# Kernel tuning notes

Hardware: AMD Instinct MI355X
Metric: run time of the kernel (lower is better)

## Reference

```python
import jax, jax.numpy as jnp
import numpy as np


def setup_inputs() -> dict:
    key = jax.random.key(0)
    ks = jax.random.split(key, 4)
    B, T, E, H = 4, 4096, 512, 64
    x = jax.random.normal(ks[0], (B, T, E), dtype=jnp.float32)
    s = 1.0 / np.sqrt(E)
    Wq = jax.random.normal(ks[1], (E, H), dtype=jnp.float32) * s
    Wk = jax.random.normal(ks[2], (E, H), dtype=jnp.float32) * s
    Wv = jax.random.normal(ks[3], (E, H), dtype=jnp.float32) * s
    bq = jnp.zeros((H,), dtype=jnp.float32)
    bk = jnp.zeros((H,), dtype=jnp.float32)
    bv = jnp.zeros((H,), dtype=jnp.float32)
    return {"x": x, "Wq": Wq, "bq": bq, "Wk": Wk, "bk": bk, "Wv": Wv, "bv": bv}


def reference(x, Wq, bq, Wk, bk, Wv, bv):
    # Single-head causal attention (masked=True path; dropout off / eval mode).
    B, T, E = x.shape
    H = Wq.shape[1]
    q = x @ Wq + bq                      # [B,T,H]
    k = x @ Wk + bk                      # [B,T,H]
    v = x @ Wv + bv                      # [B,T,H]
    scale = jnp.asarray(H, x.dtype) ** -0.5
    w = jnp.einsum('bqh,bkh->bqk', q, k) * scale   # [B,T,T]
    causal = jnp.tril(jnp.ones((T, T), dtype=bool))
    w = jnp.where(causal, w, jnp.asarray(-jnp.inf, w.dtype))
    w = jax.nn.softmax(w, axis=-1)
    out = jnp.einsum('bqk,bkh->bqh', w, v)          # [B,T,H]
    return out
```

## Files before the change

kernel.cpp:

```cpp
#include <hip/hip_runtime.h>
#include <math.h>

#define B_SZ   4
#define T_SEQ  4096
#define E_DIM  512
#define H_DIM  64
#define AW     8
#define XSTR   520
#define QSCALE 0.180336878f

typedef float f32x4 __attribute__((ext_vector_type(4)));
typedef short s16x4 __attribute__((ext_vector_type(4)));
typedef short s16x8 __attribute__((ext_vector_type(8)));
typedef unsigned int u32x4 __attribute__((ext_vector_type(4)));

static __device__ __forceinline__ unsigned short f2bf(float f) {
    union { float f; unsigned int u; } c; c.f = f;
    return (unsigned short)((c.u + 0x7fffu + ((c.u >> 16) & 1u)) >> 16);
}

static __device__ __forceinline__ float exp2f_hw(float x) {
    return __builtin_amdgcn_exp2f(x);
}

static __device__ __forceinline__ unsigned int pack_bf16(float a, float b) {
    unsigned int ua = __builtin_bit_cast(unsigned int, a) + 0x8000u;
    unsigned int ub = __builtin_bit_cast(unsigned int, b) + 0x8000u;
    return __builtin_amdgcn_perm(ub, ua, 0x07060302u);
}

__global__ __launch_bounds__(256) void wconv(
    const float* __restrict__ Wq, const float* __restrict__ Wk, const float* __restrict__ Wv,
    unsigned short* __restrict__ Wf)
{
    const int fid  = blockIdx.x * 256 + threadIdx.x;
    const int nt   = fid >> 10;
    const int kc32 = (fid >> 6) & 15;
    const int lane = fid & 63;
    const int l15  = lane & 15, g = lane >> 4;
    const int col  = nt * 16 + l15;
    const int m    = col >> 6, h = col & 63;
    const float* src = (m == 0) ? Wq : (m == 1) ? Wk : Wv;
    const float sc = (m == 0) ? QSCALE : 1.0f;
    const int k0 = kc32 * 32 + 4 * g;
    s16x8 o;
    #pragma unroll
    for (int j = 0; j < 4; ++j) {
        o[j]     = (short)f2bf(src[(k0 + j) * H_DIM + h] * sc);
        o[4 + j] = (short)f2bf(src[(k0 + 16 + j) * H_DIM + h] * sc);
    }
    *(s16x8*)(Wf + (long long)fid * 8) = o;
}

__global__ __launch_bounds__(256) void qkv_mfma(
    const float* __restrict__ x, const unsigned short* __restrict__ Wf,
    const float* __restrict__ bq, const float* __restrict__ bk, const float* __restrict__ bv,
    unsigned short* __restrict__ qf, unsigned short* __restrict__ kf,
    unsigned short* __restrict__ vf)
{
    __shared__ unsigned short Xf[2][16 * XSTR];
    __shared__ unsigned short Wout[192][36];

    const int t = threadIdx.x, wv = t >> 6, l = t & 63, l15 = l & 15, g = l >> 4;
    const long long row0 = (long long)blockIdx.x * 32;

    const float* xbase = x + row0 * E_DIM;
    #pragma unroll
    for (int i = 0; i < 16; ++i) {
        const int n = t + 256 * i;
        const int r = n >> 7;
        const int c = (n & 127) * 4;
        const f32x4 xv = *(const f32x4*)(xbase + r * E_DIM + c);
        const int rs = r >> 4, rr = r & 15;
        const int kc32 = c >> 5, rem = c & 31;
        const int gg = (rem & 15) >> 2, half = rem >> 4;
        unsigned int* dst = (unsigned int*)&Xf[rs][kc32 * XSTR + (rr + 16 * gg) * 8 + half * 4];
        dst[0] = pack_bf16(xv[0], xv[1]);
        dst[1] = pack_bf16(xv[2], xv[3]);
    }
    __syncthreads();

    f32x4 acc[2][3];
    #pragma unroll
    for (int rs = 0; rs < 2; ++rs)
        #pragma unroll
        for (int i = 0; i < 3; ++i) acc[rs][i] = (f32x4){0.f, 0.f, 0.f, 0.f};

    #pragma unroll
    for (int kc32 = 0; kc32 < 16; ++kc32) {
        const s16x8 xf0 = *(const s16x8*)&Xf[0][kc32 * XSTR + l * 8];
        const s16x8 xf1 = *(const s16x8*)&Xf[1][kc32 * XSTR + l * 8];
        #pragma unroll
        for (int i = 0; i < 3; ++i) {
            const int nt = wv + 4 * i;
            const s16x8 wf = *(const s16x8*)(Wf + (long long)((nt * 16 + kc32) * 64 + l) * 8);
            acc[0][i] = __builtin_amdgcn_mfma_f32_16x16x32_bf16(wf, xf0, acc[0][i], 0, 0, 0);
            acc[1][i] = __builtin_amdgcn_mfma_f32_16x16x32_bf16(wf, xf1, acc[1][i], 0, 0, 0);
        }
    }

    #pragma unroll
    for (int i = 0; i < 3; ++i) {
        const int nt = wv + 4 * i;
        const float* bsrc = (i == 0) ? bq : (i == 1) ? bk : bv;
        const float bscale = (i == 0) ? QSCALE : 1.0f;
        const f32x4 bb = *(const f32x4*)(bsrc + wv * 16 + 4 * g);
        #pragma unroll
        for (int rs = 0; rs < 2; ++rs)
            #pragma unroll
            for (int r = 0; r < 4; ++r)
                Wout[nt * 16 + 4 * g + r][16 * rs + l15] = f2bf(acc[rs][i][r] + bb[r] * bscale);
    }
    __syncthreads();

    #pragma unroll
    for (int rt = 0; rt < 2; ++rt) {
        const long long qt = (long long)blockIdx.x * 2 + rt;

        if (t < 128) {
            const int hc = t >> 6, ll = t & 63, p15 = ll & 15, pg = (ll >> 4);
            s16x8 o;
            #pragma unroll
            for (int j = 0; j < 4; ++j) {
                o[j]     = (short)Wout[32 * hc + 4 * pg + j][16 * rt + p15];
                o[4 + j] = (short)Wout[32 * hc + 16 + 4 * pg + j][16 * rt + p15];
            }
            *(s16x8*)(qf + qt * 1024 + hc * 512 + ll * 8) = o;
        } else {
            const int tt = t - 128, half = tt >> 6, ll = tt & 63, p15 = ll & 15, pg = (ll >> 4);
            s16x8 o;
            #pragma unroll
            for (int j = 0; j < 4; ++j) {
                o[j]     = (short)Wout[64 + 32 * half + 4 * pg + j][16 * rt + p15];
                o[4 + j] = (short)Wout[64 + 32 * half + 16 + 4 * pg + j][16 * rt + p15];
            }
            *(s16x8*)(kf + qt * 1024 + half * 512 + ll * 8) = o;
        }

        {
            const int hc = t >> 6, ll = t & 63, p15 = ll & 15, pg = (ll >> 4);
            const long long ktg = qt >> 2;
            const int half = (int)((qt >> 1) & 1), pi = (int)(qt & 1);
            s16x4 o;
            #pragma unroll
            for (int j = 0; j < 4; ++j)
                o[j] = (short)Wout[128 + hc * 16 + p15][16 * rt + 4 * pg + j];
            *(s16x4*)(vf + ktg * 4096 + hc * 1024 + half * 512 + ll * 8 + pi * 4) = o;
        }
    }
}

__global__ __launch_bounds__(512, 2) void attn(
    const unsigned short* __restrict__ qf,
    const unsigned short* __restrict__ kf,
    const unsigned short* __restrict__ vf,
    float* __restrict__ out)
{
    __shared__ float Osh[AW][64][33];
    __shared__ float msh[AW][32];
    __shared__ float lsh[AW][32];

    const int t = threadIdx.x, wv = t >> 6, l = t & 63, l15 = l & 15, g = l >> 4;

    const int bid = blockIdx.x;
    const int xcd = bid & 7;
    const int b   = xcd >> 1;
    const int u   = (bid >> 3) * 2 + (xcd & 1);
    const int qi  = 127 - u;
    const int q0  = qi * 32;
    const int adiag = (q0 + 31) >> 6;

    const unsigned short* kfb = kf + (long long)b * 64 * 4096 + l * 8;
    const unsigned short* vfb = vf + (long long)b * 64 * 4096 + l * 8;

    s16x8 Qf[2][2];
    #pragma unroll
    for (int s = 0; s < 2; ++s) {
        const unsigned short* qp = qf + ((long long)b * 256 + qi * 2 + s) * 1024 + l * 8;
        Qf[s][0] = *(const s16x8*)qp;
        Qf[s][1] = *(const s16x8*)(qp + 512);
    }

    f32x4 O[2][4];
    #pragma unroll
    for (int s = 0; s < 2; ++s)
        #pragma unroll
        for (int hc = 0; hc < 4; ++hc) O[s][hc] = (f32x4){0.f, 0.f, 0.f, 0.f};
    float m[2]   = {-INFINITY, -INFINITY};
    float lsm[2] = {0.f, 0.f};

    s16x8 Ka[4], Kc[4];
    #define LOAD_K(KT, A, C)                                              \
        {                                                                 \
            const unsigned short* p_ = kfb + (long long)(KT) * 4096;      \
            _Pragma("unroll")                                             \
            for (int ks = 0; ks < 4; ++ks) {                              \
                (A)[ks] = *(const s16x8*)(p_ + ks * 1024);                \
                (C)[ks] = *(const s16x8*)(p_ + ks * 1024 + 512);          \
            }                                                             \
        }

    if (wv <= adiag) LOAD_K(wv, Ka, Kc);

    for (int kt = wv; kt <= adiag; kt += AW) {
        const int ktb = kt * 64;
        const f32x4 z = {0.f, 0.f, 0.f, 0.f};

        f32x4 S[2][4];
        __builtin_amdgcn_s_setprio(1);
        #pragma unroll
        for (int ks = 0; ks < 4; ++ks) {
            #pragma unroll
            for (int s = 0; s < 2; ++s) {
                f32x4 s0 = __builtin_amdgcn_mfma_f32_16x16x32_bf16(Ka[ks], Qf[s][0], z, 0, 0, 0);
                S[s][ks] = __builtin_amdgcn_mfma_f32_16x16x32_bf16(Kc[ks], Qf[s][1], s0, 0, 0, 0);
            }
        }
        __builtin_amdgcn_s_setprio(0);

        s16x8 Va[4], Vc[4];
        {
            const unsigned short* pv = vfb + (long long)kt * 4096;
            #pragma unroll
            for (int hc = 0; hc < 4; ++hc) {
                Va[hc] = *(const s16x8*)(pv + hc * 1024);
                Vc[hc] = *(const s16x8*)(pv + hc * 1024 + 512);
            }
        }

        s16x8 Kna[4], Knc[4];
        const int ktn = kt + AW;
        if (ktn <= adiag) LOAD_K(ktn, Kna, Knc);

        if (kt == adiag) {
            #pragma unroll
            for (int s = 0; s < 2; ++s) {
                const int qg = q0 + 16 * s + l15;
                #pragma unroll
                for (int ks = 0; ks < 4; ++ks)
                    #pragma unroll
                    for (int r = 0; r < 4; ++r) {
                        const int key = ktb + 16 * ks + 4 * g + r;
                        S[s][ks][r] = (key > qg) ? -INFINITY : S[s][ks][r];
                    }
            }
        }

        s16x8 Pf[2][2];
        #pragma unroll
        for (int s = 0; s < 2; ++s) {
            float tm = S[s][0][0];
            #pragma unroll
            for (int ks = 0; ks < 4; ++ks)
                #pragma unroll
                for (int r = 0; r < 4; ++r) tm = fmaxf(tm, S[s][ks][r]);

            if (!__all(tm - m[s] <= 8.f)) {
                float tr = fmaxf(tm, __shfl_xor(tm, 16));
                tr = fmaxf(tr, __shfl_xor(tr, 32));
                const float mn = fmaxf(m[s], tr);
                const float alpha = exp2f_hw(m[s] - mn);
                lsm[s] *= alpha;
                #pragma unroll
                for (int hc = 0; hc < 4; ++hc) O[s][hc] *= alpha;
                m[s] = mn;
            }

            float ps = 0.f;
            #pragma unroll
            for (int ks = 0; ks < 4; ++ks)
                #pragma unroll
                for (int r = 0; r < 4; ++r) {
                    const float pp = exp2f_hw(S[s][ks][r] - m[s]);
                    S[s][ks][r] = pp;
                    ps += pp;
                }
            lsm[s] += ps;

            #pragma unroll
            for (int kc = 0; kc < 2; ++kc) {
                u32x4 w;
                #pragma unroll
                for (int i = 0; i < 4; ++i)
                    w[i] = pack_bf16(S[s][2 * kc + (i >> 1)][2 * (i & 1)],
                                     S[s][2 * kc + (i >> 1)][2 * (i & 1) + 1]);
                Pf[s][kc] = __builtin_bit_cast(s16x8, w);
            }
        }

        __builtin_amdgcn_s_setprio(1);
        #pragma unroll
        for (int hc = 0; hc < 4; ++hc) {
            #pragma unroll
            for (int s = 0; s < 2; ++s) {
                O[s][hc] = __builtin_amdgcn_mfma_f32_16x16x32_bf16(Va[hc], Pf[s][0], O[s][hc], 0, 0, 0);
                O[s][hc] = __builtin_amdgcn_mfma_f32_16x16x32_bf16(Vc[hc], Pf[s][1], O[s][hc], 0, 0, 0);
            }
        }
        __builtin_amdgcn_s_setprio(0);

        #pragma unroll
        for (int ks = 0; ks < 4; ++ks) { Ka[ks] = Kna[ks]; Kc[ks] = Knc[ks]; }
    }
    #undef LOAD_K

    #pragma unroll
    for (int s = 0; s < 2; ++s) {
        lsm[s] += __shfl_xor(lsm[s], 16);
        lsm[s] += __shfl_xor(lsm[s], 32);
    }

    #pragma unroll
    for (int s = 0; s < 2; ++s)
        #pragma unroll
        for (int hc = 0; hc < 4; ++hc)
            #pragma unroll
            for (int r = 0; r < 4; ++r)
                Osh[wv][hc * 16 + 4 * g + r][16 * s + l15] = O[s][hc][r];
    if (g == 0) {
        msh[wv][l15]      = m[0];
        msh[wv][16 + l15] = m[1];
        lsh[wv][l15]      = lsm[0];
        lsh[wv][16 + l15] = lsm[1];
    }
    __syncthreads();

    const int rl = t >> 4;
    const int h0 = (t & 15) * 4;
    float mstar = msh[0][rl];
    #pragma unroll
    for (int w = 1; w < AW; ++w) mstar = fmaxf(mstar, msh[w][rl]);
    float fw[AW], lstar = 0.f;
    #pragma unroll
    for (int w = 0; w < AW; ++w) {
        fw[w] = exp2f_hw(msh[w][rl] - mstar);
        lstar += lsh[w][rl] * fw[w];
    }
    const float inv = 1.f / lstar;

    f32x4 o0;
    #pragma unroll
    for (int j = 0; j < 4; ++j) {
        float a0 = 0.f;
        #pragma unroll
        for (int w = 0; w < AW; ++w) a0 += Osh[w][h0 + j][rl] * fw[w];
        o0[j] = a0 * inv;
    }
    *(f32x4*)(out + ((long long)b * T_SEQ + q0 + rl) * H_DIM + h0) = o0;
}

extern "C" void kernel_launch(void* const* d_in, const int* in_sizes, int n_in,
                              void* d_out, int out_size, void* d_ws, size_t ws_size,
                              hipStream_t stream) {
    const float* x  = (const float*)d_in[0];
    const float* Wq = (const float*)d_in[1];
    const float* bq = (const float*)d_in[2];
    const float* Wk = (const float*)d_in[3];
    const float* bk = (const float*)d_in[4];
    const float* Wv = (const float*)d_in[5];
    const float* bv = (const float*)d_in[6];

    const long long rows = (long long)B_SZ * T_SEQ;
    unsigned short* qfb = (unsigned short*)d_ws;
    unsigned short* kfb = qfb + rows * H_DIM;
    unsigned short* vfb = kfb + rows * H_DIM;
    unsigned short* Wfb = vfb + rows * H_DIM;

    wconv<<<dim3(48), dim3(256), 0, stream>>>(Wq, Wk, Wv, Wfb);
    qkv_mfma<<<dim3(rows / 32), dim3(256), 0, stream>>>(x, Wfb, bq, bk, bv, qfb, kfb, vfb);
    attn<<<dim3(B_SZ * 128), dim3(512), 0, stream>>>(qfb, kfb, vfb, (float*)d_out);
}
```

Before: 41.82 us.

## Share K/V tiles via double-buffered LDS across two query groups per block

The attention block now covers 64 queries (two 32-row groups of 4 waves each) instead of 32, and halves the grid. Key/value tiles are staged cooperatively into a 128KB double-buffered LDS ring, so each tile loaded from global memory is reused by both query groups, replacing per-wave direct global loads. This roughly halves global K/V traffic but adds a block-wide barrier per step. It also reduces occupancy to one block per CU and leaves only 256 blocks, which risks load imbalance on the causal triangle.

```diff
diff --git a/kernel.cpp b/kernel.cpp
--- a/kernel.cpp
+++ b/kernel.cpp
@@ -5,7 +5,6 @@
 #define T_SEQ  4096
 #define E_DIM  512
 #define H_DIM  64
-#define AW     8
 #define XSTR   520
 #define QSCALE 0.180336878f
 
@@ -150,33 +149,35 @@
     }
 }
 
-__global__ __launch_bounds__(512, 2) void attn(
+__global__ __launch_bounds__(512, 1) void attn(
     const unsigned short* __restrict__ qf,
     const unsigned short* __restrict__ kf,
     const unsigned short* __restrict__ vf,
     float* __restrict__ out)
 {
-    __shared__ float Osh[AW][64][33];
-    __shared__ float msh[AW][32];
-    __shared__ float lsh[AW][32];
+    __shared__ __align__(16) char raw[131072];
+    __shared__ float msh[2][4][32];
+    __shared__ float lsh[2][4][32];
 
     const int t = threadIdx.x, wv = t >> 6, l = t & 63, l15 = l & 15, g = l >> 4;
+    const int qg = wv >> 2, j = wv & 3;
 
     const int bid = blockIdx.x;
     const int xcd = bid & 7;
     const int b   = xcd >> 1;
     const int u   = (bid >> 3) * 2 + (xcd & 1);
-    const int qi  = 127 - u;
-    const int q0  = qi * 32;
-    const int adiag = (q0 + 31) >> 6;
-
-    const unsigned short* kfb = kf + (long long)b * 64 * 4096 + l * 8;
-    const unsigned short* vfb = vf + (long long)b * 64 * 4096 + l * 8;
+    const int qi  = 63 - u;
+    const int q0  = qi * 64;
+    const int adiag = qi;
+
+    const unsigned short* kfb = kf + (long long)b * 64 * 4096;
+    const unsigned short* vfb = vf + (long long)b * 64 * 4096;
+    const unsigned short* sfb = qg ? vfb : kfb;
 
     s16x8 Qf[2][2];
     #pragma unroll
     for (int s = 0; s < 2; ++s) {
-        const unsigned short* qp = qf + ((long long)b * 256 + qi * 2 + s) * 1024 + l * 8;
+        const unsigned short* qp = qf + ((long long)b * 256 + qi * 4 + qg * 2 + s) * 1024 + l * 8;
         Qf[s][0] = *(const s16x8*)qp;
         Qf[s][1] = *(const s16x8*)(qp + 512);
     }
@@ -189,120 +190,135 @@
     float m[2]   = {-INFINITY, -INFINITY};
     float lsm[2] = {0.f, 0.f};
 
-    s16x8 Ka[4], Kc[4];
-    #define LOAD_K(KT, A, C)                                              \
-        {                                                                 \
-            const unsigned short* p_ = kfb + (long long)(KT) * 4096;      \
-            _Pragma("unroll")                                             \
-            for (int ks = 0; ks < 4; ++ks) {                              \
-                (A)[ks] = *(const s16x8*)(p_ + ks * 1024);                \
-                (C)[ks] = *(const s16x8*)(p_ + ks * 1024 + 512);          \
-            }                                                             \
-        }
-
-    if (wv <= adiag) LOAD_K(wv, Ka, Kc);
-
-    for (int kt = wv; kt <= adiag; kt += AW) {
-        const int ktb = kt * 64;
-        const f32x4 z = {0.f, 0.f, 0.f, 0.f};
-
-        f32x4 S[2][4];
-        __builtin_amdgcn_s_setprio(1);
-        #pragma unroll
-        for (int ks = 0; ks < 4; ++ks) {
+    if (j <= adiag) {
+        const unsigned short* src = sfb + (long long)j * 4096 + l * 8;
+        char* dst = raw + j * 16384 + qg * 8192 + l * 16;
+        #pragma unroll
+        for (int c = 0; c < 8; ++c)
+            *(u32x4*)(dst + c * 1024) = *(const u32x4*)(src + c * 512);
+    }
+    __syncthreads();
+
+    const int N = adiag / 4 + 1;
+    for (int n = 0; n < N; ++n) {
+        const int cur = n & 1;
+
+        u32x4 stg[8];
+        const int kt2 = 4 * (n + 1) + j;
+        const bool do_stage = (kt2 <= adiag);
+        if (do_stage) {
+            const unsigned short* src = sfb + (long long)kt2 * 4096 + l * 8;
+            #pragma unroll
+            for (int c = 0; c < 8; ++c) stg[c] = *(const u32x4*)(src + c * 512);
+        }
+
+        const int kt = 4 * n + j;
+        if (kt <= adiag) {
+            const char* slot = raw + ((cur << 2) | j) * 16384 + l * 16;
+            const int ktb = kt * 64;
+            const f32x4 z = {0.f, 0.f, 0.f, 0.f};
+
+            s16x8 Ka[4], Kc[4];
+            #pragma unroll
+            for (int ks = 0; ks < 4; ++ks) {
+                Ka[ks] = *(const s16x8*)(slot + ks * 2048);
+                Kc[ks] = *(const s16x8*)(slot + ks * 2048 + 1024);
+            }
+
+            f32x4 S[2][4];
+            __builtin_amdgcn_s_setprio(1);
+            #pragma unroll
+            for (int ks = 0; ks < 4; ++ks) {
+                #pragma unroll
+                for (int s = 0; s < 2; ++s) {
+                    f32x4 s0 = __builtin_amdgcn_mfma_f32_16x16x32_bf16(Ka[ks], Qf[s][0], z, 0, 0, 0);
+                    S[s][ks] = __builtin_amdgcn_mfma_f32_16x16x32_bf16(Kc[ks], Qf[s][1], s0, 0, 0, 0);
+                }
+            }
+            __builtin_amdgcn_s_setprio(0);
+
+            s16x8 Va[4], Vc[4];
+            #pragma unroll
+            for (int hc = 0; hc < 4; ++hc) {
+                Va[hc] = *(const s16x8*)(slot + 8192 + hc * 2048);
+                Vc[hc] = *(const s16x8*)(slot + 8192 + hc * 2048 + 1024);
+            }
+
+            if (kt == adiag) {
+                #pragma unroll
+                for (int s = 0; s < 2; ++s) {
+                    const int qg_row = q0 + 32 * qg + 16 * s + l15;
+                    #pragma unroll
+                    for (int ks = 0; ks < 4; ++ks)
+                        #pragma unroll
+                        for (int r = 0; r < 4; ++r) {
+                            const int key = ktb + 16 * ks + 4 * g + r;
+                            S[s][ks][r] = (key > qg_row) ? -INFINITY : S[s][ks][r];
+                        }
+                }
+            }
+
+            s16x8 Pf[2][2];
             #pragma unroll
             for (int s = 0; s < 2; ++s) {
-                f32x4 s0 = __builtin_amdgcn_mfma_f32_16x16x32_bf16(Ka[ks], Qf[s][0], z, 0, 0, 0);
-                S[s][ks] = __builtin_amdgcn_mfma_f32_16x16x32_bf16(Kc[ks], Qf[s][1], s0, 0, 0, 0);
-            }
-        }
-        __builtin_amdgcn_s_setprio(0);
-
-        s16x8 Va[4], Vc[4];
-        {
-            const unsigned short* pv = vfb + (long long)kt * 4096;
+                float tm = S[s][0][0];
+                #pragma unroll
+                for (int ks = 0; ks < 4; ++ks)
+                    #pragma unroll
+                    for (int r = 0; r < 4; ++r) tm = fmaxf(tm, S[s][ks][r]);
+
+                if (!__all(tm - m[s] <= 8.f)) {
+                    float tr = fmaxf(tm, __shfl_xor(tm, 16));
+                    tr = fmaxf(tr, __shfl_xor(tr, 32));
+                    const float mn = fmaxf(m[s], tr);
+                    const float alpha = exp2f_hw(m[s] - mn);
+                    lsm[s] *= alpha;
+                    #pragma unroll
+                    for (int hc = 0; hc < 4; ++hc) O[s][hc] *= alpha;
+                    m[s] = mn;
+                }
+
+                float ps = 0.f;
+                #pragma unroll
+                for (int ks = 0; ks < 4; ++ks)
+                    #pragma unroll
+                    for (int r = 0; r < 4; ++r) {
+                        const float pp = exp2f_hw(S[s][ks][r] - m[s]);
+                        S[s][ks][r] = pp;
+                        ps += pp;
+                    }
+                lsm[s] += ps;
+
+                #pragma unroll
+                for (int kc = 0; kc < 2; ++kc) {
+                    u32x4 w;
+                    #pragma unroll
+                    for (int i = 0; i < 4; ++i)
+                        w[i] = pack_bf16(S[s][2 * kc + (i >> 1)][2 * (i & 1)],
+                                         S[s][2 * kc + (i >> 1)][2 * (i & 1) + 1]);
+                    Pf[s][kc] = __builtin_bit_cast(s16x8, w);
+                }
+            }
+
+            __builtin_amdgcn_s_setprio(1);
             #pragma unroll
             for (int hc = 0; hc < 4; ++hc) {
-                Va[hc] = *(const s16x8*)(pv + hc * 1024);
-                Vc[hc] = *(const s16x8*)(pv + hc * 1024 + 512);
-            }
-        }
-
-        s16x8 Kna[4], Knc[4];
-        const int ktn = kt + AW;
-        if (ktn <= adiag) LOAD_K(ktn, Kna, Knc);
-
-        if (kt == adiag) {
-            #pragma unroll
-            for (int s = 0; s < 2; ++s) {
-                const int qg = q0 + 16 * s + l15;
-                #pragma unroll
-                for (int ks = 0; ks < 4; ++ks)
-                    #pragma unroll
-                    for (int r = 0; r < 4; ++r) {
-                        const int key = ktb + 16 * ks + 4 * g + r;
-                        S[s][ks][r] = (key > qg) ? -INFINITY : S[s][ks][r];
-                    }
-            }
-        }
-
-        s16x8 Pf[2][2];
-        #pragma unroll
-        for (int s = 0; s < 2; ++s) {
-            float tm = S[s][0][0];
-            #pragma unroll
-            for (int ks = 0; ks < 4; ++ks)
-                #pragma unroll
-                for (int r = 0; r < 4; ++r) tm = fmaxf(tm, S[s][ks][r]);
-
-            if (!__all(tm - m[s] <= 8.f)) {
-                float tr = fmaxf(tm, __shfl_xor(tm, 16));
-                tr = fmaxf(tr, __shfl_xor(tr, 32));
-                const float mn = fmaxf(m[s], tr);
-                const float alpha = exp2f_hw(m[s] - mn);
-                lsm[s] *= alpha;
-                #pragma unroll
-                for (int hc = 0; hc < 4; ++hc) O[s][hc] *= alpha;
-                m[s] = mn;
-            }
-
-            float ps = 0.f;
-            #pragma unroll
-            for (int ks = 0; ks < 4; ++ks)
-                #pragma unroll
-                for (int r = 0; r < 4; ++r) {
-                    const float pp = exp2f_hw(S[s][ks][r] - m[s]);
-                    S[s][ks][r] = pp;
-                    ps += pp;
-                }
-            lsm[s] += ps;
-
-            #pragma unroll
-            for (int kc = 0; kc < 2; ++kc) {
-                u32x4 w;
-                #pragma unroll
-                for (int i = 0; i < 4; ++i)
-                    w[i] = pack_bf16(S[s][2 * kc + (i >> 1)][2 * (i & 1)],
-                                     S[s][2 * kc + (i >> 1)][2 * (i & 1) + 1]);
-                Pf[s][kc] = __builtin_bit_cast(s16x8, w);
-            }
-        }
-
-        __builtin_amdgcn_s_setprio(1);
-        #pragma unroll
-        for (int hc = 0; hc < 4; ++hc) {
-            #pragma unroll
-            for (int s = 0; s < 2; ++s) {
-                O[s][hc] = __builtin_amdgcn_mfma_f32_16x16x32_bf16(Va[hc], Pf[s][0], O[s][hc], 0, 0, 0);
-                O[s][hc] = __builtin_amdgcn_mfma_f32_16x16x32_bf16(Vc[hc], Pf[s][1], O[s][hc], 0, 0, 0);
-            }
-        }
-        __builtin_amdgcn_s_setprio(0);
-
-        #pragma unroll
-        for (int ks = 0; ks < 4; ++ks) { Ka[ks] = Kna[ks]; Kc[ks] = Knc[ks]; }
-    }
-    #undef LOAD_K
+                #pragma unroll
+                for (int s = 0; s < 2; ++s) {
+                    O[s][hc] = __builtin_amdgcn_mfma_f32_16x16x32_bf16(Va[hc], Pf[s][0], O[s][hc], 0, 0, 0);
+                    O[s][hc] = __builtin_amdgcn_mfma_f32_16x16x32_bf16(Vc[hc], Pf[s][1], O[s][hc], 0, 0, 0);
+                }
+            }
+            __builtin_amdgcn_s_setprio(0);
+        }
+
+        if (do_stage) {
+            char* dst = raw + (((cur ^ 1) << 2) | j) * 16384 + qg * 8192 + l * 16;
+            #pragma unroll
+            for (int c = 0; c < 8; ++c) *(u32x4*)(dst + c * 1024) = stg[c];
+        }
+        __syncthreads();
+    }
 
     #pragma unroll
     for (int s = 0; s < 2; ++s) {
@@ -310,43 +326,53 @@
         lsm[s] += __shfl_xor(lsm[s], 32);
     }
 
+    float* OshG = (float*)(raw + qg * 36864);
     #pragma unroll
     for (int s = 0; s < 2; ++s)
         #pragma unroll
         for (int hc = 0; hc < 4; ++hc)
             #pragma unroll
             for (int r = 0; r < 4; ++r)
-                Osh[wv][hc * 16 + 4 * g + r][16 * s + l15] = O[s][hc][r];
+                OshG[j * 2112 + (hc * 16 + 4 * g + r) * 33 + 16 * s + l15] = O[s][hc][r];
     if (g == 0) {
-        msh[wv][l15]      = m[0];
-        msh[wv][16 + l15] = m[1];
-        lsh[wv][l15]      = lsm[0];
-        lsh[wv][16 + l15] = lsm[1];
+        msh[qg][j][l15]      = m[0];
+        msh[qg][j][16 + l15] = m[1];
+        lsh[qg][j][l15]      = lsm[0];
+        lsh[qg][j][16 + l15] = lsm[1];
     }
     __syncthreads();
 
-    const int rl = t >> 4;
-    const int h0 = (t & 15) * 4;
-    float mstar = msh[0][rl];
-    #pragma unroll
-    for (int w = 1; w < AW; ++w) mstar = fmaxf(mstar, msh[w][rl]);
-    float fw[AW], lstar = 0.f;
-    #pragma unroll
-    for (int w = 0; w < AW; ++w) {
-        fw[w] = exp2f_hw(msh[w][rl] - mstar);
-        lstar += lsh[w][rl] * fw[w];
+    const int qg2 = t >> 8, tt = t & 255;
+    const int rl = tt >> 3;
+    const int h0 = (tt & 7) * 8;
+    const float* OshR = (const float*)(raw + qg2 * 36864);
+
+    float mstar = msh[qg2][0][rl];
+    #pragma unroll
+    for (int w = 1; w < 4; ++w) mstar = fmaxf(mstar, msh[qg2][w][rl]);
+    float fw[4], lstar = 0.f;
+    #pragma unroll
+    for (int w = 0; w < 4; ++w) {
+        fw[w] = exp2f_hw(msh[qg2][w][rl] - mstar);
+        lstar += lsh[qg2][w][rl] * fw[w];
     }
     const float inv = 1.f / lstar;
 
-    f32x4 o0;
-    #pragma unroll
-    for (int j = 0; j < 4; ++j) {
-        float a0 = 0.f;
-        #pragma unroll
-        for (int w = 0; w < AW; ++w) a0 += Osh[w][h0 + j][rl] * fw[w];
-        o0[j] = a0 * inv;
-    }
-    *(f32x4*)(out + ((long long)b * T_SEQ + q0 + rl) * H_DIM + h0) = o0;
+    f32x4 o0, o1;
+    #pragma unroll
+    for (int jj = 0; jj < 4; ++jj) {
+        float a0 = 0.f, a1 = 0.f;
+        #pragma unroll
+        for (int w = 0; w < 4; ++w) {
+            a0 += OshR[w * 2112 + (h0 + jj) * 33 + rl] * fw[w];
+            a1 += OshR[w * 2112 + (h0 + 4 + jj) * 33 + rl] * fw[w];
+        }
+        o0[jj] = a0 * inv;
+        o1[jj] = a1 * inv;
+    }
+    float* op = out + ((long long)b * T_SEQ + q0 + qg2 * 32 + rl) * H_DIM + h0;
+    *(f32x4*)op = o0;
+    *(f32x4*)(op + 4) = o1;
 }
 
 extern "C" void kernel_launch(void* const* d_in, const int* in_sizes, int n_in,
@@ -368,5 +394,5 @@
 
     wconv<<<dim3(48), dim3(256), 0, stream>>>(Wq, Wk, Wv, Wfb);
     qkv_mfma<<<dim3(rows / 32), dim3(256), 0, stream>>>(x, Wfb, bq, bk, bv, qfb, kfb, vfb);
-    attn<<<dim3(B_SZ * 128), dim3(512), 0, stream>>>(qfb, kfb, vfb, (float*)d_out);
-}
+    attn<<<dim3(B_SZ * 64), dim3(512), 0, stream>>>(qfb, kfb, vfb, (float*)d_out);
+}
```

Result: slower. 56.91 us (+36.1%).
